# Kernel tuning notes

Hardware: AMD Instinct MI355X
Metric: run time of the kernel (lower is better)

## Reference

```python
import jax, jax.numpy as jnp
import numpy as np

J, XD, HD, YD, P, N = 64, 512, 1024, 16, 8, 1024


def setup_inputs() -> dict:
    key = jax.random.key(0)
    ks = jax.random.split(key, 14)
    b1 = 2.0 / np.sqrt(XD)
    b2 = 2.0 / np.sqrt(HD)
    rng = np.random.RandomState(0)
    # stack of P permutation matrices [P, YD, YD]
    permu = jnp.asarray(np.stack([np.eye(YD, dtype=np.float32)[rng.permutation(YD)] for _ in range(P)]))
    return {
        "x": jax.random.normal(ks[0], (N, XD), jnp.float32),
        "mu_W1": b1 * (jax.random.uniform(ks[1], (XD, HD)) - 0.5),
        "mu_b1": b1 * (jax.random.uniform(ks[2], (1, HD)) - 0.5),
        "mu_W2": b2 * (jax.random.uniform(ks[3], (HD, YD)) - 0.5),
        "mu_b2": b2 * (jax.random.uniform(ks[4], (1, YD)) - 0.5),
        "sig_W1": b1 * jax.random.uniform(ks[5], (XD, HD)),
        "sig_b1": b1 * jax.random.uniform(ks[6], (1, HD)),
        "sig_W2": b2 * jax.random.uniform(ks[7], (HD, YD)),
        "sig_b2": b2 * jax.random.uniform(ks[8], (1, YD)),
        "e_W1": jax.random.normal(ks[9], (J, XD, HD), jnp.float32),
        "e_b1": jax.random.normal(ks[10], (J, 1, HD), jnp.float32),
        "e_W2": jax.random.normal(ks[11], (J, HD, YD), jnp.float32),
        "e_b2": jax.random.normal(ks[12], (J, 1, YD), jnp.float32),
        "permu": permu,
    }


def reference(x, mu_W1, mu_b1, mu_W2, mu_b2, sig_W1, sig_b1, sig_W2, sig_b2,
              e_W1, e_b1, e_W2, e_b2, permu):
    # reparameterized weight samples: [J, ...]
    W1 = mu_W1 + e_W1 * sig_W1          # [J, XD, HD]
    b1 = mu_b1 + e_b1 * sig_b1          # [J, 1, HD]
    W2 = mu_W2 + e_W2 * sig_W2          # [J, HD, YD]
    b2 = mu_b2 + e_b2 * sig_b2          # [J, 1, YD]
    xf = x.reshape(-1, XD)
    # Hardtanh(-1, 1) == clip
    h = jnp.clip(jnp.einsum('nx,jxh->jnh', xf, W1) + b1, -1.0, 1.0)  # [J, N, HD]
    out = jnp.einsum('jnh,jhy->jny', h, W2) + b2                      # [J, N, YD]
    all_out = jnp.einsum('jnc,pcy->jpny', out, permu)                 # [J, P, N, YD]
    return all_out.reshape(J * P, xf.shape[0], YD)
```

## Files before the change

### kernel.cpp

```cpp
#include <hip/hip_runtime.h>
#include <cstdint>
#include <cstddef>

#define J 64
#define XD 512
#define HD 1024
#define YD 16
#define PP 8
#define NN 1024

typedef __bf16 bf16;
typedef __attribute__((ext_vector_type(8))) __bf16 bf16x8;
typedef __attribute__((ext_vector_type(4))) __bf16 bf16x4;
typedef __attribute__((ext_vector_type(4))) float f32x4;

__device__ __forceinline__ void gload16(const void* g, void* l) {
  __builtin_amdgcn_global_load_lds((__attribute__((address_space(1))) void*)(g),
                                   (__attribute__((address_space(3))) void*)(l),
                                   16, 0, 0);
}

__global__ __launch_bounds__(256) void build_w1t(
    const float* __restrict__ muW1, const float* __restrict__ sigW1,
    const float* __restrict__ eW1, bf16* __restrict__ W1T) {
  __shared__ bf16 sT[64][66];
  int b = blockIdx.x;
  int j = b >> 7;
  int xt = (b >> 4) & 7;
  int ht = b & 15;
  int x0 = xt << 6, h0 = ht << 6;
  int tid = threadIdx.x;
  int rp = tid >> 4;
  int cp = (tid & 15) << 2;
  const float* eB = eW1 + (size_t)j * (XD * HD);
#pragma unroll
  for (int p = 0; p < 4; ++p) {
    int x = rp + (p << 4);
    size_t gi = (size_t)(x0 + x) * HD + (h0 + cp);
    f32x4 e = *(const f32x4*)(eB + gi);
    f32x4 m = *(const f32x4*)(muW1 + gi);
    f32x4 s = *(const f32x4*)(sigW1 + gi);
#pragma unroll
    for (int i = 0; i < 4; ++i) sT[cp + i][x] = (bf16)(m[i] + e[i] * s[i]);
  }
  __syncthreads();
#pragma unroll
  for (int p = 0; p < 4; ++p) {
    int h = rp + (p << 4);
    bf16x4 v;
#pragma unroll
    for (int i = 0; i < 4; ++i) v[i] = sT[h][cp + i];
    *(bf16x4*)(W1T + (size_t)(j * HD + h0 + h) * XD + (x0 + cp)) = v;
  }
}

__global__ __launch_bounds__(256) void build_small(
    const float* __restrict__ x,
    const float* __restrict__ muW2, const float* __restrict__ sigW2,
    const float* __restrict__ eW2,
    const float* __restrict__ mub1, const float* __restrict__ sigb1,
    const float* __restrict__ eb1,
    const float* __restrict__ mub2, const float* __restrict__ sigb2,
    const float* __restrict__ eb2,
    bf16* __restrict__ XBF, bf16* __restrict__ W2T,
    float* __restrict__ B1W, float* __restrict__ B2W) {
  int i = blockIdx.x * 256 + threadIdx.x;
  const int c0 = NN * XD;
  const int c1 = J * YD * HD;
  const int c2 = J * HD;
  const int c3 = J * YD;
  if (i < c0) { XBF[i] = (bf16)x[i]; return; }
  i -= c0;
  if (i < c1) {
    int h = i & (HD - 1);
    int jy = i >> 10;
    int y = jy & 15;
    int j = jy >> 4;
    float mu = muW2[h * YD + y], sg = sigW2[h * YD + y];
    float e = eW2[((size_t)j * HD + h) * YD + y];
    W2T[i] = (bf16)(mu + e * sg);
    return;
  }
  i -= c1;
  if (i < c2) {
    int h = i & (HD - 1);
    B1W[i] = mub1[h] + eb1[i] * sigb1[h];
    return;
  }
  i -= c2;
  if (i < c3) {
    int y = i & 15;
    B2W[i] = mub2[y] + eb2[i] * sigb2[y];
  }
}

__global__ __launch_bounds__(256)
void fused_mlp(
    const bf16* __restrict__ XBF, const bf16* __restrict__ W1T,
    const bf16* __restrict__ W2T, const float* __restrict__ B1W,
    const float* __restrict__ B2W, const float* __restrict__ permu,
    float* __restrict__ out) {
  extern __shared__ char smem[];

  int bid = blockIdx.x;
  int L = ((bid & 7) << 6) | (bid >> 3);
  int j = L >> 3;
  int n0 = (L & 7) << 7;

  int tid = threadIdx.x;
  int wid = tid >> 6;
  int lane = tid & 63;
  int l15 = lane & 15;
  int lg = lane >> 4;
  int wh = wid << 6;

  const bf16* w1base = W1T + (size_t)j * (HD * XD);
  const bf16* w2g = W2T + (size_t)((j << 4) + l15) * HD;
  bf16* sH = (bf16*)(smem + 49152);

  f32x4 acc2[2];
#pragma unroll
  for (int f = 0; f < 2; ++f)
#pragma unroll
    for (int r = 0; r < 4; ++r) acc2[f][r] = 0.0f;

  auto stage = [&](int d, int k0, int hb_) {
#pragma unroll
    for (int q = 0; q < 2; ++q) {
      int doff = (q << 12) + (tid << 4);
      int pr = doff >> 7;
      int sl = ((doff >> 4) & 7) ^ (pr & 7);
      int n = (pr << 1) | (sl >> 2);
      int kc = sl & 3;
      gload16(XBF + (size_t)(n0 + n) * XD + k0 + (kc << 3),
              smem + d * 8192 + doff);
    }
#pragma unroll
    for (int q = 0; q < 4; ++q) {
      int doff = (q << 12) + (tid << 4);
      int pr = doff >> 7;
      int sl = ((doff >> 4) & 7) ^ (pr & 7);
      int h = (pr << 1) | (sl >> 2);
      int kc = sl & 3;
      gload16(w1base + (size_t)((hb_ << 8) + h) * XD + k0 + (kc << 3),
              smem + 16384 + d * 16384 + doff);
    }
  };

  stage(0, 0, 0);
  asm volatile("s_waitcnt vmcnt(0)" ::: "memory");
  __builtin_amdgcn_s_barrier();

#pragma unroll 1
  for (int hb = 0; hb < 4; ++hb) {
    f32x4 acc1[4][8];
#pragma unroll
    for (int fb = 0; fb < 4; ++fb)
#pragma unroll
      for (int fa = 0; fa < 8; ++fa)
#pragma unroll
        for (int r = 0; r < 4; ++r) acc1[fb][fa][r] = 0.0f;

#pragma unroll 1
    for (int t = 0; t < 16; ++t) {
      int s = (hb << 4) + t;
      int cur = s & 1;
      if (t < 15)           stage(cur ^ 1, (t + 1) << 5, hb);
      else if (hb < 3)      stage(cur ^ 1, 0, hb + 1);
      const char* a_d = smem + cur * 8192;
      const char* b_d = smem + 16384 + cur * 16384;
      bf16x8 af[8], bg[4];
#pragma unroll
      for (int fa = 0; fa < 8; ++fa) {
        int n = (fa << 4) + l15;
        int pr = n >> 1;
        int ph = (((n & 1) << 2) | lg) ^ (pr & 7);
        af[fa] = *(const bf16x8*)(a_d + (pr << 7) + (ph << 4));
      }
#pragma unroll
      for (int fb = 0; fb < 4; ++fb) {
        int h = wh + (fb << 4) + l15;
        int pr = h >> 1;
        int ph = (((h & 1) << 2) | lg) ^ (pr & 7);
        bg[fb] = *(const bf16x8*)(b_d + (pr << 7) + (ph << 4));
      }
      __builtin_amdgcn_s_setprio(1);
#pragma unroll
      for (int fb = 0; fb < 4; ++fb)
#pragma unroll
        for (int fa = 0; fa < 8; ++fa)
          acc1[fb][fa] = __builtin_amdgcn_mfma_f32_16x16x32_bf16(
              bg[fb], af[fa], acc1[fb][fa], 0, 0, 0);
      __builtin_amdgcn_s_setprio(0);
      asm volatile("s_waitcnt vmcnt(0)" ::: "memory");
      __builtin_amdgcn_s_barrier();
    }

    f32x4 b1v[4];
#pragma unroll
    for (int fb = 0; fb < 4; ++fb)
      b1v[fb] = *(const f32x4*)&B1W[(j << 10) + (hb << 8) + wh + (fb << 4) + (lg << 2)];

#pragma unroll 1
    for (int c = 0; c < 2; ++c) {
      __builtin_amdgcn_s_barrier();
      bf16x8 wg[4];
#pragma unroll
      for (int kk2 = 0; kk2 < 4; ++kk2)
        wg[kk2] = *(const bf16x8*)(w2g + (hb << 8) + (c << 7) + (kk2 << 5) + (lg << 3));
      if ((wid >> 1) == c) {
#pragma unroll
        for (int fa = 0; fa < 8; ++fa)
#pragma unroll
          for (int fb = 0; fb < 4; ++fb) {
            bf16x4 pk;
#pragma unroll
            for (int r = 0; r < 4; ++r) {
              float v = acc1[fb][fa][r] + b1v[fb][r];
              v = fminf(1.0f, fmaxf(-1.0f, v));
              pk[r] = (bf16)v;
            }
            int n = (fa << 4) + l15;
            int hl = ((wid & 1) << 6) + (fb << 4) + (lg << 2);
            int byte = (n << 8) + ((hl << 1) ^ ((n & 7) << 4));
            *(bf16x4*)((char*)sH + byte) = pk;
          }
      }
      asm volatile("s_waitcnt lgkmcnt(0)" ::: "memory");
      __builtin_amdgcn_s_barrier();
#pragma unroll
      for (int kk2 = 0; kk2 < 4; ++kk2) {
#pragma unroll
        for (int f = 0; f < 2; ++f) {
          int row = (wid << 5) + (f << 4) + l15;
          int cb = ((kk2 << 6) + (lg << 4)) ^ ((row & 7) << 4);
          bf16x8 hf = *(const bf16x8*)((char*)sH + (row << 8) + cb);
          acc2[f] = __builtin_amdgcn_mfma_f32_16x16x32_bf16(hf, wg[kk2], acc2[f], 0, 0, 0);
        }
      }
    }
  }

  float b2v = B2W[(j << 4) + l15];
  float* sOut = (float*)smem;
  int* sIdx = (int*)(smem + 20480);
#pragma unroll
  for (int f = 0; f < 2; ++f)
#pragma unroll
    for (int r = 0; r < 4; ++r) {
      int row = (wid << 5) + (f << 4) + (lg << 2) + r;
      sOut[row * 17 + l15] = acc2[f][r] + b2v;
    }
  if (tid < 128) {
    int p = tid >> 4, y = tid & 15;
    int c = 0;
#pragma unroll
    for (int cc = 0; cc < 16; ++cc)
      if (permu[((p << 4) + cc) * 16 + y] > 0.5f) c = cc;
    sIdx[tid] = c;
  }
  __syncthreads();
#pragma unroll 1
  for (int it = 0; it < 16; ++it) {
    int flat = (it << 10) + (tid << 2);
    int p = flat >> 11;
    int n = (flat >> 4) & 127;
    int y0 = flat & 15;
    f32x4 v;
#pragma unroll
    for (int q = 0; q < 4; ++q) v[q] = sOut[n * 17 + sIdx[(p << 4) + y0 + q]];
    *(f32x4*)(out + ((size_t)((j << 3) + p) * NN + n0 + n) * YD + y0) = v;
  }
}

extern "C" void kernel_launch(void* const* d_in, const int* in_sizes, int n_in,
                              void* d_out, int out_size, void* d_ws, size_t ws_size,
                              hipStream_t stream) {
  (void)in_sizes; (void)n_in; (void)out_size; (void)ws_size;
  const float* x      = (const float*)d_in[0];
  const float* mu_W1  = (const float*)d_in[1];
  const float* mu_b1  = (const float*)d_in[2];
  const float* mu_W2  = (const float*)d_in[3];
  const float* mu_b2  = (const float*)d_in[4];
  const float* sig_W1 = (const float*)d_in[5];
  const float* sig_b1 = (const float*)d_in[6];
  const float* sig_W2 = (const float*)d_in[7];
  const float* sig_b2 = (const float*)d_in[8];
  const float* e_W1   = (const float*)d_in[9];
  const float* e_b1   = (const float*)d_in[10];
  const float* e_W2   = (const float*)d_in[11];
  const float* e_b2   = (const float*)d_in[12];
  const float* permu  = (const float*)d_in[13];
  float* out = (float*)d_out;

  char* ws = (char*)d_ws;
  bf16* W1T = (bf16*)(ws);
  bf16* W2T = (bf16*)(ws + 67108864);
  bf16* XBF = (bf16*)(ws + 69206016);
  float* B1W = (float*)(ws + 70254592);
  float* B2W = (float*)(ws + 70516736);

  static int lds_set = 0;
  if (!lds_set) {
    hipFuncSetAttribute((const void*)fused_mlp,
                        hipFuncAttributeMaxDynamicSharedMemorySize, 81920);
    lds_set = 1;
  }

  build_w1t<<<dim3(8192), dim3(256), 0, stream>>>(mu_W1, sig_W1, e_W1, W1T);
  build_small<<<dim3(6404), dim3(256), 0, stream>>>(
      x, mu_W2, sig_W2, e_W2, mu_b1, sig_b1, e_b1, mu_b2, sig_b2, e_b2,
      XBF, W2T, B1W, B2W);
  fused_mlp<<<dim3(512), dim3(256), 81920, stream>>>(
      XBF, W1T, W2T, B1W, B2W, permu, out);
}
```

Before: 147.4 us.

## Merge build kernels and retile fused MLP warps to a 2x2 grid

Merges the W1-transpose build kernel and the small-parameter build kernel into one launch, with each block branching on its index. In the fused MLP, the four warps now tile the 128x256 per-step product as a 2x2 grid (64 rows by 128 hidden units each) instead of each warp owning all rows and 64 hidden units. This halves the A-fragment LDS reads per warp, and the hidden-activation staging buffer shrinks so the second GEMM runs in four 64-wide chunks. LDS drops from 80 KB to 64 KB, and the tile loads for the current step are issued before the next stage prefetch. The cost is more barriers in the second-GEMM loop, and the hipFuncSetAttribute call is removed.

```diff
diff --git a/kernel.cpp b/kernel.cpp
--- a/kernel.cpp
+++ b/kernel.cpp
@@ -20,41 +20,9 @@
                                    16, 0, 0);
 }
 
-__global__ __launch_bounds__(256) void build_w1t(
+__global__ __launch_bounds__(256) void build_all(
     const float* __restrict__ muW1, const float* __restrict__ sigW1,
-    const float* __restrict__ eW1, bf16* __restrict__ W1T) {
-  __shared__ bf16 sT[64][66];
-  int b = blockIdx.x;
-  int j = b >> 7;
-  int xt = (b >> 4) & 7;
-  int ht = b & 15;
-  int x0 = xt << 6, h0 = ht << 6;
-  int tid = threadIdx.x;
-  int rp = tid >> 4;
-  int cp = (tid & 15) << 2;
-  const float* eB = eW1 + (size_t)j * (XD * HD);
-#pragma unroll
-  for (int p = 0; p < 4; ++p) {
-    int x = rp + (p << 4);
-    size_t gi = (size_t)(x0 + x) * HD + (h0 + cp);
-    f32x4 e = *(const f32x4*)(eB + gi);
-    f32x4 m = *(const f32x4*)(muW1 + gi);
-    f32x4 s = *(const f32x4*)(sigW1 + gi);
-#pragma unroll
-    for (int i = 0; i < 4; ++i) sT[cp + i][x] = (bf16)(m[i] + e[i] * s[i]);
-  }
-  __syncthreads();
-#pragma unroll
-  for (int p = 0; p < 4; ++p) {
-    int h = rp + (p << 4);
-    bf16x4 v;
-#pragma unroll
-    for (int i = 0; i < 4; ++i) v[i] = sT[h][cp + i];
-    *(bf16x4*)(W1T + (size_t)(j * HD + h0 + h) * XD + (x0 + cp)) = v;
-  }
-}
-
-__global__ __launch_bounds__(256) void build_small(
+    const float* __restrict__ eW1, bf16* __restrict__ W1T,
     const float* __restrict__ x,
     const float* __restrict__ muW2, const float* __restrict__ sigW2,
     const float* __restrict__ eW2,
@@ -64,7 +32,39 @@
     const float* __restrict__ eb2,
     bf16* __restrict__ XBF, bf16* __restrict__ W2T,
     float* __restrict__ B1W, float* __restrict__ B2W) {
-  int i = blockIdx.x * 256 + threadIdx.x;
+  __shared__ bf16 sT[64][66];
+  int b = blockIdx.x;
+  int tid = threadIdx.x;
+  if (b < 8192) {
+    int j = b >> 7;
+    int xt = (b >> 4) & 7;
+    int ht = b & 15;
+    int x0 = xt << 6, h0 = ht << 6;
+    int rp = tid >> 4;
+    int cp = (tid & 15) << 2;
+    const float* eB = eW1 + (size_t)j * (XD * HD);
+#pragma unroll
+    for (int p = 0; p < 4; ++p) {
+      int xx = rp + (p << 4);
+      size_t gi = (size_t)(x0 + xx) * HD + (h0 + cp);
+      f32x4 e = *(const f32x4*)(eB + gi);
+      f32x4 m = *(const f32x4*)(muW1 + gi);
+      f32x4 s = *(const f32x4*)(sigW1 + gi);
+#pragma unroll
+      for (int i = 0; i < 4; ++i) sT[cp + i][xx] = (bf16)(m[i] + e[i] * s[i]);
+    }
+    __syncthreads();
+#pragma unroll
+    for (int p = 0; p < 4; ++p) {
+      int h = rp + (p << 4);
+      bf16x4 v;
+#pragma unroll
+      for (int i = 0; i < 4; ++i) v[i] = sT[h][cp + i];
+      *(bf16x4*)(W1T + (size_t)(j * HD + h0 + h) * XD + (x0 + cp)) = v;
+    }
+    return;
+  }
+  int i = (b - 8192) * 256 + tid;
   const int c0 = NN * XD;
   const int c1 = J * YD * HD;
   const int c2 = J * HD;
@@ -112,7 +112,8 @@
   int lane = tid & 63;
   int l15 = lane & 15;
   int lg = lane >> 4;
-  int wh = wid << 6;
+  int wn2 = (wid & 1) << 6;
+  int wh2 = (wid >> 1) << 7;
 
   const bf16* w1base = W1T + (size_t)j * (HD * XD);
   const bf16* w2g = W2T + (size_t)((j << 4) + l15) * HD;
@@ -153,42 +154,41 @@
 
 #pragma unroll 1
   for (int hb = 0; hb < 4; ++hb) {
-    f32x4 acc1[4][8];
-#pragma unroll
-    for (int fb = 0; fb < 4; ++fb)
-#pragma unroll
-      for (int fa = 0; fa < 8; ++fa)
+    f32x4 acc1[8][4];
+#pragma unroll
+    for (int fb = 0; fb < 8; ++fb)
+#pragma unroll
+      for (int fa = 0; fa < 4; ++fa)
 #pragma unroll
         for (int r = 0; r < 4; ++r) acc1[fb][fa][r] = 0.0f;
 
 #pragma unroll 1
     for (int t = 0; t < 16; ++t) {
-      int s = (hb << 4) + t;
-      int cur = s & 1;
+      int cur = ((hb << 4) + t) & 1;
+      const char* a_d = smem + cur * 8192;
+      const char* b_d = smem + 16384 + cur * 16384;
+      bf16x8 af[4], bg[8];
+#pragma unroll
+      for (int fa = 0; fa < 4; ++fa) {
+        int ra = wn2 + (fa << 4) + l15;
+        int pr = ra >> 1;
+        int ph = (((ra & 1) << 2) | lg) ^ (pr & 7);
+        af[fa] = *(const bf16x8*)(a_d + (pr << 7) + (ph << 4));
+      }
+#pragma unroll
+      for (int fb = 0; fb < 8; ++fb) {
+        int rb = wh2 + (fb << 4) + l15;
+        int pr = rb >> 1;
+        int ph = (((rb & 1) << 2) | lg) ^ (pr & 7);
+        bg[fb] = *(const bf16x8*)(b_d + (pr << 7) + (ph << 4));
+      }
       if (t < 15)           stage(cur ^ 1, (t + 1) << 5, hb);
       else if (hb < 3)      stage(cur ^ 1, 0, hb + 1);
-      const char* a_d = smem + cur * 8192;
-      const char* b_d = smem + 16384 + cur * 16384;
-      bf16x8 af[8], bg[4];
-#pragma unroll
-      for (int fa = 0; fa < 8; ++fa) {
-        int n = (fa << 4) + l15;
-        int pr = n >> 1;
-        int ph = (((n & 1) << 2) | lg) ^ (pr & 7);
-        af[fa] = *(const bf16x8*)(a_d + (pr << 7) + (ph << 4));
-      }
-#pragma unroll
-      for (int fb = 0; fb < 4; ++fb) {
-        int h = wh + (fb << 4) + l15;
-        int pr = h >> 1;
-        int ph = (((h & 1) << 2) | lg) ^ (pr & 7);
-        bg[fb] = *(const bf16x8*)(b_d + (pr << 7) + (ph << 4));
-      }
       __builtin_amdgcn_s_setprio(1);
 #pragma unroll
-      for (int fb = 0; fb < 4; ++fb)
-#pragma unroll
-        for (int fa = 0; fa < 8; ++fa)
+      for (int fb = 0; fb < 8; ++fb)
+#pragma unroll
+        for (int fa = 0; fa < 4; ++fa)
           acc1[fb][fa] = __builtin_amdgcn_mfma_f32_16x16x32_bf16(
               bg[fb], af[fa], acc1[fb][fa], 0, 0, 0);
       __builtin_amdgcn_s_setprio(0);
@@ -196,23 +196,24 @@
       __builtin_amdgcn_s_barrier();
     }
 
-    f32x4 b1v[4];
-#pragma unroll
-    for (int fb = 0; fb < 4; ++fb)
-      b1v[fb] = *(const f32x4*)&B1W[(j << 10) + (hb << 8) + wh + (fb << 4) + (lg << 2)];
-
-#pragma unroll 1
-    for (int c = 0; c < 2; ++c) {
+    f32x4 b1v[8];
+#pragma unroll
+    for (int fb = 0; fb < 8; ++fb)
+      b1v[fb] = *(const f32x4*)&B1W[(j << 10) + (hb << 8) + wh2 + (fb << 4) + (lg << 2)];
+
+#pragma unroll
+    for (int c = 0; c < 4; ++c) {
       __builtin_amdgcn_s_barrier();
-      bf16x8 wg[4];
-#pragma unroll
-      for (int kk2 = 0; kk2 < 4; ++kk2)
-        wg[kk2] = *(const bf16x8*)(w2g + (hb << 8) + (c << 7) + (kk2 << 5) + (lg << 3));
-      if ((wid >> 1) == c) {
-#pragma unroll
-        for (int fa = 0; fa < 8; ++fa)
-#pragma unroll
-          for (int fb = 0; fb < 4; ++fb) {
+      bf16x8 wg[2];
+#pragma unroll
+      for (int k2 = 0; k2 < 2; ++k2)
+        wg[k2] = *(const bf16x8*)(w2g + (hb << 8) + (c << 6) + (k2 << 5) + (lg << 3));
+      if ((wid >> 1) == (c >> 1)) {
+#pragma unroll
+        for (int fa = 0; fa < 4; ++fa)
+#pragma unroll
+          for (int q = 0; q < 4; ++q) {
+            int fb = ((c & 1) << 2) + q;
             bf16x4 pk;
 #pragma unroll
             for (int r = 0; r < 4; ++r) {
@@ -220,22 +221,22 @@
               v = fminf(1.0f, fmaxf(-1.0f, v));
               pk[r] = (bf16)v;
             }
-            int n = (fa << 4) + l15;
-            int hl = ((wid & 1) << 6) + (fb << 4) + (lg << 2);
-            int byte = (n << 8) + ((hl << 1) ^ ((n & 7) << 4));
+            int n = wn2 + (fa << 4) + l15;
+            int hl = (q << 4) + (lg << 2);
+            int byte = (n << 7) + ((hl << 1) ^ ((n & 7) << 4));
             *(bf16x4*)((char*)sH + byte) = pk;
           }
       }
       asm volatile("s_waitcnt lgkmcnt(0)" ::: "memory");
       __builtin_amdgcn_s_barrier();
 #pragma unroll
-      for (int kk2 = 0; kk2 < 4; ++kk2) {
+      for (int k2 = 0; k2 < 2; ++k2) {
 #pragma unroll
         for (int f = 0; f < 2; ++f) {
           int row = (wid << 5) + (f << 4) + l15;
-          int cb = ((kk2 << 6) + (lg << 4)) ^ ((row & 7) << 4);
-          bf16x8 hf = *(const bf16x8*)((char*)sH + (row << 8) + cb);
-          acc2[f] = __builtin_amdgcn_mfma_f32_16x16x32_bf16(hf, wg[kk2], acc2[f], 0, 0, 0);
+          int cb = ((k2 << 6) + (lg << 4)) ^ ((row & 7) << 4);
+          bf16x8 hf = *(const bf16x8*)((char*)sH + (row << 7) + cb);
+          acc2[f] = __builtin_amdgcn_mfma_f32_16x16x32_bf16(hf, wg[k2], acc2[f], 0, 0, 0);
         }
       }
     }
@@ -243,7 +244,7 @@
 
   float b2v = B2W[(j << 4) + l15];
   float* sOut = (float*)smem;
-  int* sIdx = (int*)(smem + 20480);
+  int* sIdx = (int*)(smem + 12288);
 #pragma unroll
   for (int f = 0; f < 2; ++f)
 #pragma unroll
@@ -300,17 +301,10 @@
   float* B1W = (float*)(ws + 70254592);
   float* B2W = (float*)(ws + 70516736);
 
-  static int lds_set = 0;
-  if (!lds_set) {
-    hipFuncSetAttribute((const void*)fused_mlp,
-                        hipFuncAttributeMaxDynamicSharedMemorySize, 81920);
-    lds_set = 1;
-  }
-
-  build_w1t<<<dim3(8192), dim3(256), 0, stream>>>(mu_W1, sig_W1, e_W1, W1T);
-  build_small<<<dim3(6404), dim3(256), 0, stream>>>(
+  build_all<<<dim3(14596), dim3(256), 0, stream>>>(
+      mu_W1, sig_W1, e_W1, W1T,
       x, mu_W2, sig_W2, e_W2, mu_b1, sig_b1, e_b1, mu_b2, sig_b2, e_b2,
       XBF, W2T, B1W, B2W);
-  fused_mlp<<<dim3(512), dim3(256), 81920, stream>>>(
+  fused_mlp<<<dim3(512), dim3(256), 65536, stream>>>(
       XBF, W1T, W2T, B1W, B2W, permu, out);
 }
```

After: 149.4 us. No clear change (+1.4%).
